# Kernel tuning notes

Hardware: AMD Instinct MI355X
Metric: run time of the kernel (lower is better)

## Reference

```python
import jax, jax.numpy as jnp
import numpy as np

N_NODES = 50000
N_GRAPHS = 64
HID = 128
IN_DIM = 128
N_LAYERS = 3


def setup_inputs() -> dict:
    key = jax.random.key(0)
    ks = jax.random.split(key, 12)
    x = jax.random.normal(ks[0], (N_NODES, IN_DIM), dtype=jnp.float32)
    edge_index = jax.random.randint(ks[1], (2, 800000), 0, N_NODES, dtype=jnp.int64)
    batch = jnp.sort(jax.random.randint(ks[2], (N_NODES,), 0, N_GRAPHS, dtype=jnp.int64))
    s = 1.0 / np.sqrt(HID)
    W0 = jax.random.normal(ks[3], (IN_DIM, HID), dtype=jnp.float32) * s
    b0 = jnp.zeros((HID,), dtype=jnp.float32)
    Ws = jax.random.normal(ks[4], (N_LAYERS, HID, HID), dtype=jnp.float32) * s
    bs = jnp.zeros((N_LAYERS, HID), dtype=jnp.float32)
    W1 = jax.random.normal(ks[5], (HID, HID // 2), dtype=jnp.float32) * s
    b1 = jnp.zeros((HID // 2,), dtype=jnp.float32)
    W2 = jax.random.normal(ks[6], (HID // 2, 2), dtype=jnp.float32) * (1.0 / np.sqrt(HID // 2))
    b2 = jnp.zeros((2,), dtype=jnp.float32)
    return {"x": x, "edge_index": edge_index, "batch": batch,
            "W0": W0, "b0": b0, "Ws": Ws, "bs": bs,
            "W1": W1, "b1": b1, "W2": W2, "b2": b2}


def reference(x, edge_index, batch, W0, b0, Ws, bs, W1, b1, W2, b2):
    n = x.shape[0]
    # GCN: add self-loops, symmetric normalization D^-1/2 (A+I) D^-1/2
    loop = jnp.arange(n, dtype=edge_index.dtype)
    src = jnp.concatenate([edge_index[0], loop])  # [E+N]
    dst = jnp.concatenate([edge_index[1], loop])
    deg = jax.ops.segment_sum(jnp.ones_like(dst, dtype=x.dtype), dst, num_segments=n)
    dinv = jax.lax.rsqrt(jnp.maximum(deg, 1.0))
    coef = (dinv[src] * dinv[dst])[:, None]  # [E+N, 1]

    def gcn(h, W, b):
        hw = h @ W                                  # transform first (cheaper)
        agg = jax.ops.segment_sum(hw[src] * coef, dst, num_segments=n)
        return jax.nn.relu(agg + b)

    h = gcn(x, W0, b0)
    for i in range(Ws.shape[0]):
        h = gcn(h, Ws[i], bs[i])

    # global mean pool over graphs
    sums = jax.ops.segment_sum(h, batch, num_segments=N_GRAPHS)
    cnts = jax.ops.segment_sum(jnp.ones((n,), dtype=h.dtype), batch, num_segments=N_GRAPHS)
    pooled = sums / jnp.maximum(cnts, 1.0)[:, None]  # [G, HID]

    out = jax.nn.relu(pooled @ W1 + b1) @ W2 + b2    # [G, 2]
    return out
```

## Files before the change

### kernel.cpp

```cpp
#include <hip/hip_runtime.h>
#include <hip/hip_bf16.h>
#include <hip/hip_fp16.h>

#define HID 128
#define N_GRAPHS 64

__global__ void init_deg_kernel(int* __restrict__ deg, int n) {
    int i = blockIdx.x * 256 + threadIdx.x;
    if (i < n) deg[i] = 1;
}

__global__ void count_kernel(const int* __restrict__ dst, int* __restrict__ deg, int E) {
    int e = blockIdx.x * 256 + threadIdx.x;
    if (e < E) atomicAdd(&deg[dst[e]], 1);
}

__global__ __launch_bounds__(256) void scan_partial_kernel(const int* __restrict__ deg,
                                                           int* __restrict__ bsum, int n) {
    __shared__ int red[256];
    int t = threadIdx.x;
    int i = blockIdx.x * 256 + t;
    red[t] = (i < n) ? deg[i] : 0;
    __syncthreads();
#pragma unroll
    for (int s = 128; s > 0; s >>= 1) {
        if (t < s) red[t] += red[t + s];
        __syncthreads();
    }
    if (t == 0) bsum[blockIdx.x] = red[0];
}

__global__ __launch_bounds__(256) void scan_bsum_kernel(const int* __restrict__ bsum,
                                                        int* __restrict__ boff,
                                                        int* __restrict__ row_ptr,
                                                        int nb, int n) {
    __shared__ int arr[256];
    int t = threadIdx.x;
    int own = (t < nb) ? bsum[t] : 0;
    arr[t] = own;
    __syncthreads();
#pragma unroll
    for (int off = 1; off < 256; off <<= 1) {
        int v = arr[t];
        int add = (t >= off) ? arr[t - off] : 0;
        __syncthreads();
        arr[t] = v + add;
        __syncthreads();
    }
    if (t < nb) boff[t] = arr[t] - own;
    if (t == 255) row_ptr[n] = arr[255];
}

__global__ __launch_bounds__(256) void scan_emit_kernel(const int* __restrict__ deg,
                                                        const int* __restrict__ boff,
                                                        int* __restrict__ row_ptr,
                                                        int* __restrict__ cursor,
                                                        float* __restrict__ dinv, int n) {
    __shared__ int arr[256];
    int t = threadIdx.x;
    int i = blockIdx.x * 256 + t;
    int d = (i < n) ? deg[i] : 0;
    arr[t] = d;
    __syncthreads();
#pragma unroll
    for (int off = 1; off < 256; off <<= 1) {
        int v = arr[t];
        int add = (t >= off) ? arr[t - off] : 0;
        __syncthreads();
        arr[t] = v + add;
        __syncthreads();
    }
    if (i < n) {
        int pos = boff[blockIdx.x] + arr[t] - d;
        row_ptr[i] = pos;
        cursor[i] = pos;
        dinv[i] = rsqrtf((float)d);
    }
}

__global__ void fill_kernel(const int* __restrict__ src, const int* __restrict__ dst,
                            int* __restrict__ cursor, int* __restrict__ col,
                            int E, int EN) {
    int e = blockIdx.x * 256 + threadIdx.x;
    if (e >= EN) return;
    int s, d;
    if (e < E) { s = src[e]; d = dst[e]; }
    else       { s = e - E; d = s; }
    int pos = atomicAdd(&cursor[d], 1);
    col[pos] = s;
}

__global__ __launch_bounds__(256) void gemm_scale_kernel(const float* __restrict__ A,
                                                         const float* __restrict__ W,
                                                         const float* __restrict__ dinv,
                                                         __half* __restrict__ out16, int M) {
    __shared__ float sAT[2][32][68];
    __shared__ float sW [2][32][132];
    int tid = threadIdx.x;
    int row0 = blockIdx.x * 64;
    int ty = tid >> 5, tx = tid & 31;
    int r0 = ty * 8;
    int j0 = tx * 4;

    float acc[8][4];
#pragma unroll
    for (int i = 0; i < 8; ++i)
#pragma unroll
        for (int j = 0; j < 4; ++j) acc[i][j] = 0.f;

#pragma unroll
    for (int p = 0; p < 4; ++p) {
        int idx = tid + p * 256;
        int k = idx >> 5, c4 = idx & 31;
        *(float4*)&sW[0][k][c4 * 4] = *(const float4*)(W + (size_t)k * 128 + c4 * 4);
    }
#pragma unroll
    for (int p = 0; p < 2; ++p) {
        int idx = tid + p * 256;
        int r = idx >> 3, c4 = idx & 7;
        float4 v = make_float4(0.f, 0.f, 0.f, 0.f);
        if (row0 + r < M) v = *(const float4*)(A + (size_t)(row0 + r) * 128 + c4 * 4);
        sAT[0][c4 * 4 + 0][r] = v.x;
        sAT[0][c4 * 4 + 1][r] = v.y;
        sAT[0][c4 * 4 + 2][r] = v.z;
        sAT[0][c4 * 4 + 3][r] = v.w;
    }
    __syncthreads();

    for (int kci = 0; kci < 4; ++kci) {
        int cur = kci & 1;
        float4 wreg[4], areg[2];
        if (kci < 3) {
            int kc = (kci + 1) * 32;
#pragma unroll
            for (int p = 0; p < 4; ++p) {
                int idx = tid + p * 256;
                int k = idx >> 5, c4 = idx & 31;
                wreg[p] = *(const float4*)(W + (size_t)(kc + k) * 128 + c4 * 4);
            }
#pragma unroll
            for (int p = 0; p < 2; ++p) {
                int idx = tid + p * 256;
                int r = idx >> 3, c4 = idx & 7;
                areg[p] = make_float4(0.f, 0.f, 0.f, 0.f);
                if (row0 + r < M) areg[p] = *(const float4*)(A + (size_t)(row0 + r) * 128 + kc + c4 * 4);
            }
        }

#pragma unroll 4
        for (int k = 0; k < 32; ++k) {
            float4 a0 = *(float4*)&sAT[cur][k][r0];
            float4 a1 = *(float4*)&sAT[cur][k][r0 + 4];
            float4 w4 = *(float4*)&sW[cur][k][j0];
            float a[8] = {a0.x, a0.y, a0.z, a0.w, a1.x, a1.y, a1.z, a1.w};
#pragma unroll
            for (int i = 0; i < 8; ++i) {
                acc[i][0] += a[i] * w4.x;
                acc[i][1] += a[i] * w4.y;
                acc[i][2] += a[i] * w4.z;
                acc[i][3] += a[i] * w4.w;
            }
        }
        __syncthreads();

        if (kci < 3) {
            int nbuf = cur ^ 1;
#pragma unroll
            for (int p = 0; p < 4; ++p) {
                int idx = tid + p * 256;
                int k = idx >> 5, c4 = idx & 31;
                *(float4*)&sW[nbuf][k][c4 * 4] = wreg[p];
            }
#pragma unroll
            for (int p = 0; p < 2; ++p) {
                int idx = tid + p * 256;
                int r = idx >> 3, c4 = idx & 7;
                sAT[nbuf][c4 * 4 + 0][r] = areg[p].x;
                sAT[nbuf][c4 * 4 + 1][r] = areg[p].y;
                sAT[nbuf][c4 * 4 + 2][r] = areg[p].z;
                sAT[nbuf][c4 * 4 + 3][r] = areg[p].w;
            }
            __syncthreads();
        }
    }

#pragma unroll
    for (int i = 0; i < 8; ++i) {
        int r = row0 + r0 + i;
        if (r < M) {
            float dv = dinv[r];
            __half2 h0 = __floats2half2_rn(acc[i][0] * dv, acc[i][1] * dv);
            __half2 h1 = __floats2half2_rn(acc[i][2] * dv, acc[i][3] * dv);
            float2 pk;
            ((__half2*)&pk)[0] = h0; ((__half2*)&pk)[1] = h1;
            *(float2*)(out16 + (size_t)r * 128 + j0) = pk;
        }
    }
}

__global__ __launch_bounds__(256) void aggregate_kernel(const __half* __restrict__ hw,
                                                        const int* __restrict__ row_ptr,
                                                        const int* __restrict__ col,
                                                        const float* __restrict__ dinv,
                                                        const float* __restrict__ bias,
                                                        float* __restrict__ out, int n) {
    int tid = threadIdx.x;
    int v = blockIdx.x * 16 + (tid >> 4);
    if (v >= n) return;
    int j = (tid & 15) * 8;
    int p0 = row_ptr[v], p1 = row_ptr[v + 1];
    float acc[8];
#pragma unroll
    for (int q = 0; q < 8; ++q) acc[q] = 0.f;

    int p = p0;
    for (; p + 3 < p1; p += 4) {
        int s0 = col[p], s1 = col[p + 1], s2 = col[p + 2], s3 = col[p + 3];
        float4 r0 = *(const float4*)(hw + (size_t)s0 * 128 + j);
        float4 r1 = *(const float4*)(hw + (size_t)s1 * 128 + j);
        float4 r2 = *(const float4*)(hw + (size_t)s2 * 128 + j);
        float4 r3 = *(const float4*)(hw + (size_t)s3 * 128 + j);
        const __half2* h0 = (const __half2*)&r0;
        const __half2* h1 = (const __half2*)&r1;
        const __half2* h2 = (const __half2*)&r2;
        const __half2* h3 = (const __half2*)&r3;
#pragma unroll
        for (int q = 0; q < 4; ++q) {
            float2 f0 = __half22float2(h0[q]);
            float2 f1 = __half22float2(h1[q]);
            float2 f2 = __half22float2(h2[q]);
            float2 f3 = __half22float2(h3[q]);
            acc[2 * q + 0] += (f0.x + f1.x) + (f2.x + f3.x);
            acc[2 * q + 1] += (f0.y + f1.y) + (f2.y + f3.y);
        }
    }
    for (; p < p1; ++p) {
        int s0 = col[p];
        float4 r0 = *(const float4*)(hw + (size_t)s0 * 128 + j);
        const __half2* h0 = (const __half2*)&r0;
#pragma unroll
        for (int q = 0; q < 4; ++q) {
            float2 f0 = __half22float2(h0[q]);
            acc[2 * q + 0] += f0.x;
            acc[2 * q + 1] += f0.y;
        }
    }
    float dv = dinv[v];
    float4 bb0 = *(const float4*)(bias + j);
    float4 bb1 = *(const float4*)(bias + j + 4);
    float4 o0, o1;
    o0.x = fmaxf(acc[0] * dv + bb0.x, 0.f);
    o0.y = fmaxf(acc[1] * dv + bb0.y, 0.f);
    o0.z = fmaxf(acc[2] * dv + bb0.z, 0.f);
    o0.w = fmaxf(acc[3] * dv + bb0.w, 0.f);
    o1.x = fmaxf(acc[4] * dv + bb1.x, 0.f);
    o1.y = fmaxf(acc[5] * dv + bb1.y, 0.f);
    o1.z = fmaxf(acc[6] * dv + bb1.z, 0.f);
    o1.w = fmaxf(acc[7] * dv + bb1.w, 0.f);
    *(float4*)(out + (size_t)v * 128 + j) = o0;
    *(float4*)(out + (size_t)v * 128 + j + 4) = o1;
}

__global__ void boundary_kernel(const int* __restrict__ batch, int* __restrict__ start, int n) {
    int i = blockIdx.x * 256 + threadIdx.x;
    if (i >= n) return;
    int b = batch[i];
    int pb = (i > 0) ? batch[i - 1] : -1;
    if (b != pb) {
        for (int g = pb + 1; g <= b; ++g) start[g] = i;
    }
    if (i == n - 1) {
        for (int g = b + 1; g <= N_GRAPHS; ++g) start[g] = n;
    }
}

__global__ __launch_bounds__(256) void pool_reduce_kernel(const float* __restrict__ h,
                                                          const int* __restrict__ start,
                                                          float* __restrict__ pooled) {
    __shared__ float part[8][128];
    int g = blockIdx.x;
    int s = start[g], e = start[g + 1];
    int tid = threadIdx.x;
    int grp = tid >> 5;
    int j = (tid & 31) * 4;
    float4 acc = make_float4(0.f, 0.f, 0.f, 0.f);
    for (int v = s + grp; v < e; v += 8) {
        float4 a = *(const float4*)(h + (size_t)v * 128 + j);
        acc.x += a.x; acc.y += a.y; acc.z += a.z; acc.w += a.w;
    }
    *(float4*)&part[grp][j] = acc;
    __syncthreads();
    if (tid < 128) {
        float sum = 0.f;
#pragma unroll
        for (int k = 0; k < 8; ++k) sum += part[k][tid];
        int cntv = e - s; if (cntv < 1) cntv = 1;
        pooled[g * 128 + tid] = sum / (float)cntv;
    }
}

__global__ __launch_bounds__(256) void mlp_kernel(const float* __restrict__ pooled_g,
                                                  const float* __restrict__ W1,
                                                  const float* __restrict__ b1,
                                                  const float* __restrict__ W2,
                                                  const float* __restrict__ b2,
                                                  float* __restrict__ out) {
    __shared__ float pooled[64][128];
    __shared__ float h1[64][64];
    int tid = threadIdx.x;
    for (int i = tid; i < 64 * 128; i += 256) pooled[i >> 7][i & 127] = pooled_g[i];
    __syncthreads();
    for (int i = tid; i < 64 * 64; i += 256) {
        int g = i >> 6, j = i & 63;
        float acc = b1[j];
        for (int k = 0; k < 128; ++k) acc += pooled[g][k] * W1[k * 64 + j];
        h1[g][j] = fmaxf(acc, 0.f);
    }
    __syncthreads();
    if (tid < 128) {
        int g = tid >> 1, c = tid & 1;
        float acc = b2[c];
        for (int jj = 0; jj < 64; ++jj) acc += h1[g][jj] * W2[jj * 2 + c];
        out[tid] = acc;
    }
}

extern "C" void kernel_launch(void* const* d_in, const int* in_sizes, int n_in,
                              void* d_out, int out_size, void* d_ws, size_t ws_size,
                              hipStream_t stream) {
    const float* x    = (const float*)d_in[0];
    const int*   ei   = (const int*)d_in[1];
    const int*   batch= (const int*)d_in[2];
    const float* W0   = (const float*)d_in[3];
    const float* b0   = (const float*)d_in[4];
    const float* Ws   = (const float*)d_in[5];
    const float* bs   = (const float*)d_in[6];
    const float* W1   = (const float*)d_in[7];
    const float* b1   = (const float*)d_in[8];
    const float* W2   = (const float*)d_in[9];
    const float* b2   = (const float*)d_in[10];
    float* out = (float*)d_out;

    const int n  = in_sizes[0] / HID;
    const int E  = in_sizes[1] / 2;
    const int EN = E + n;
    const int* src = ei;
    const int* dst = ei + E;
    const int nb = (n + 255) / 256;

    char* ws = (char*)d_ws;
    size_t off = 0;
    auto alloc = [&](size_t bytes) { void* p = ws + off; off = (off + bytes + 255) & ~(size_t)255; return p; };
    float*  bufA   = (float*) alloc((size_t)n * HID * 4);
    __half* hw16   = (__half*)alloc((size_t)n * HID * 2);
    float*  dinv   = (float*) alloc((size_t)n * 4);
    int*    row_ptr= (int*)   alloc((size_t)(n + 1) * 4);
    int*    cursor = (int*)   alloc((size_t)n * 4);
    int*    deg    = (int*)   alloc((size_t)n * 4);
    int*    col    = (int*)   alloc((size_t)EN * 4);
    int*    bsum   = (int*)   alloc((size_t)nb * 4);
    int*    boff   = (int*)   alloc((size_t)nb * 4);
    int*    gstart = (int*)   alloc((N_GRAPHS + 1) * 4);
    float*  pooled = (float*) alloc(N_GRAPHS * 128 * 4);
    (void)ws_size; (void)n_in; (void)out_size;

    init_deg_kernel<<<nb, 256, 0, stream>>>(deg, n);
    count_kernel<<<(E + 255) / 256, 256, 0, stream>>>(dst, deg, E);
    scan_partial_kernel<<<nb, 256, 0, stream>>>(deg, bsum, n);
    scan_bsum_kernel<<<1, 256, 0, stream>>>(bsum, boff, row_ptr, nb, n);
    scan_emit_kernel<<<nb, 256, 0, stream>>>(deg, boff, row_ptr, cursor, dinv, n);
    fill_kernel<<<(EN + 255) / 256, 256, 0, stream>>>(src, dst, cursor, col, E, EN);
    boundary_kernel<<<nb, 256, 0, stream>>>(batch, gstart, n);

    const int gemm_grid = (n + 63) / 64;
    const int node_grid = (n + 15) / 16;

    gemm_scale_kernel<<<gemm_grid, 256, 0, stream>>>(x, W0, dinv, hw16, n);
    aggregate_kernel<<<node_grid, 256, 0, stream>>>(hw16, row_ptr, col, dinv, b0, bufA, n);
    for (int l = 0; l < 3; ++l) {
        gemm_scale_kernel<<<gemm_grid, 256, 0, stream>>>(bufA, Ws + (size_t)l * HID * HID, dinv, hw16, n);
        aggregate_kernel<<<node_grid, 256, 0, stream>>>(hw16, row_ptr, col, dinv, bs + (size_t)l * HID, bufA, n);
    }

    pool_reduce_kernel<<<N_GRAPHS, 256, 0, stream>>>(bufA, gstart, pooled);
    mlp_kernel<<<1, 256, 0, stream>>>(pooled, W1, b1, W2, b2, out);
}
```

Before: 511.0 us.

## Use fp16 MFMA for node transforms and store activations in half precision

Replaces the fp32 SIMT tiled GEMM with a matrix-core kernel using mfma_f32_16x16x32_f16. W is transposed and converted to fp16 in shared memory, and each wave computes 16 rows. Layer activations are now stored as fp16, so the aggregate output, the GEMM input and the pooling all read and write half the bytes, and a conversion kernel turns x into fp16 up front. This costs precision through fp16 rounding of the inputs, the weights and the intermediate hidden states. The output stores are narrow 2-byte scattered writes.

Result: faster. 461.8 us (-9.6%).

```diff
diff --git a/kernel.cpp b/kernel.cpp
--- a/kernel.cpp
+++ b/kernel.cpp
@@ -4,6 +4,9 @@
 
 #define HID 128
 #define N_GRAPHS 64
+
+typedef _Float16 h8 __attribute__((ext_vector_type(8)));
+typedef float f4 __attribute__((ext_vector_type(4)));
 
 __global__ void init_deg_kernel(int* __restrict__ deg, int n) {
     int i = blockIdx.x * 256 + threadIdx.x;
@@ -90,110 +93,78 @@
     col[pos] = s;
 }
 
-__global__ __launch_bounds__(256) void gemm_scale_kernel(const float* __restrict__ A,
-                                                         const float* __restrict__ W,
-                                                         const float* __restrict__ dinv,
-                                                         __half* __restrict__ out16, int M) {
-    __shared__ float sAT[2][32][68];
-    __shared__ float sW [2][32][132];
+__global__ void cvt_kernel(const float* __restrict__ in, __half* __restrict__ out, int total8) {
+    int i = blockIdx.x * 256 + threadIdx.x;
+    if (i >= total8) return;
+    float4 v0 = *(const float4*)(in + (size_t)i * 8);
+    float4 v1 = *(const float4*)(in + (size_t)i * 8 + 4);
+    __half2 p0 = __floats2half2_rn(v0.x, v0.y);
+    __half2 p1 = __floats2half2_rn(v0.z, v0.w);
+    __half2 p2 = __floats2half2_rn(v1.x, v1.y);
+    __half2 p3 = __floats2half2_rn(v1.z, v1.w);
+    float4 pk;
+    ((__half2*)&pk)[0] = p0; ((__half2*)&pk)[1] = p1;
+    ((__half2*)&pk)[2] = p2; ((__half2*)&pk)[3] = p3;
+    *(float4*)(out + (size_t)i * 8) = pk;
+}
+
+__global__ __launch_bounds__(256) void gemm_mfma_kernel(const __half* __restrict__ A16,
+                                                        const float* __restrict__ W,
+                                                        const float* __restrict__ dinv,
+                                                        __half* __restrict__ out16, int M) {
+    __shared__ _Float16 sWt[128][136];
     int tid = threadIdx.x;
-    int row0 = blockIdx.x * 64;
-    int ty = tid >> 5, tx = tid & 31;
-    int r0 = ty * 8;
-    int j0 = tx * 4;
-
-    float acc[8][4];
-#pragma unroll
-    for (int i = 0; i < 8; ++i)
-#pragma unroll
-        for (int j = 0; j < 4; ++j) acc[i][j] = 0.f;
-
-#pragma unroll
-    for (int p = 0; p < 4; ++p) {
-        int idx = tid + p * 256;
-        int k = idx >> 5, c4 = idx & 31;
-        *(float4*)&sW[0][k][c4 * 4] = *(const float4*)(W + (size_t)k * 128 + c4 * 4);
-    }
-#pragma unroll
-    for (int p = 0; p < 2; ++p) {
-        int idx = tid + p * 256;
-        int r = idx >> 3, c4 = idx & 7;
-        float4 v = make_float4(0.f, 0.f, 0.f, 0.f);
-        if (row0 + r < M) v = *(const float4*)(A + (size_t)(row0 + r) * 128 + c4 * 4);
-        sAT[0][c4 * 4 + 0][r] = v.x;
-        sAT[0][c4 * 4 + 1][r] = v.y;
-        sAT[0][c4 * 4 + 2][r] = v.z;
-        sAT[0][c4 * 4 + 3][r] = v.w;
-    }
-    __syncthreads();
-
-    for (int kci = 0; kci < 4; ++kci) {
-        int cur = kci & 1;
-        float4 wreg[4], areg[2];
-        if (kci < 3) {
-            int kc = (kci + 1) * 32;
-#pragma unroll
-            for (int p = 0; p < 4; ++p) {
-                int idx = tid + p * 256;
-                int k = idx >> 5, c4 = idx & 31;
-                wreg[p] = *(const float4*)(W + (size_t)(kc + k) * 128 + c4 * 4);
-            }
-#pragma unroll
-            for (int p = 0; p < 2; ++p) {
-                int idx = tid + p * 256;
-                int r = idx >> 3, c4 = idx & 7;
-                areg[p] = make_float4(0.f, 0.f, 0.f, 0.f);
-                if (row0 + r < M) areg[p] = *(const float4*)(A + (size_t)(row0 + r) * 128 + kc + c4 * 4);
-            }
-        }
-
-#pragma unroll 4
-        for (int k = 0; k < 32; ++k) {
-            float4 a0 = *(float4*)&sAT[cur][k][r0];
-            float4 a1 = *(float4*)&sAT[cur][k][r0 + 4];
-            float4 w4 = *(float4*)&sW[cur][k][j0];
-            float a[8] = {a0.x, a0.y, a0.z, a0.w, a1.x, a1.y, a1.z, a1.w};
-#pragma unroll
-            for (int i = 0; i < 8; ++i) {
-                acc[i][0] += a[i] * w4.x;
-                acc[i][1] += a[i] * w4.y;
-                acc[i][2] += a[i] * w4.z;
-                acc[i][3] += a[i] * w4.w;
-            }
-        }
-        __syncthreads();
-
-        if (kci < 3) {
-            int nbuf = cur ^ 1;
-#pragma unroll
-            for (int p = 0; p < 4; ++p) {
-                int idx = tid + p * 256;
-                int k = idx >> 5, c4 = idx & 31;
-                *(float4*)&sW[nbuf][k][c4 * 4] = wreg[p];
-            }
-#pragma unroll
-            for (int p = 0; p < 2; ++p) {
-                int idx = tid + p * 256;
-                int r = idx >> 3, c4 = idx & 7;
-                sAT[nbuf][c4 * 4 + 0][r] = areg[p].x;
-                sAT[nbuf][c4 * 4 + 1][r] = areg[p].y;
-                sAT[nbuf][c4 * 4 + 2][r] = areg[p].z;
-                sAT[nbuf][c4 * 4 + 3][r] = areg[p].w;
-            }
-            __syncthreads();
-        }
-    }
-
-#pragma unroll
-    for (int i = 0; i < 8; ++i) {
-        int r = row0 + r0 + i;
-        if (r < M) {
-            float dv = dinv[r];
-            __half2 h0 = __floats2half2_rn(acc[i][0] * dv, acc[i][1] * dv);
-            __half2 h1 = __floats2half2_rn(acc[i][2] * dv, acc[i][3] * dv);
-            float2 pk;
-            ((__half2*)&pk)[0] = h0; ((__half2*)&pk)[1] = h1;
-            *(float2*)(out16 + (size_t)r * 128 + j0) = pk;
+    for (int i = tid * 4; i < 128 * 128; i += 1024) {
+        int k = i >> 7, nn = i & 127;
+        float4 v = *(const float4*)(W + i);
+        sWt[nn + 0][k] = (_Float16)v.x;
+        sWt[nn + 1][k] = (_Float16)v.y;
+        sWt[nn + 2][k] = (_Float16)v.z;
+        sWt[nn + 3][k] = (_Float16)v.w;
+    }
+    __syncthreads();
+
+    int wave = tid >> 6;
+    int lane = tid & 63;
+    int l15 = lane & 15;
+    int kg = lane >> 4;
+    int rowb = blockIdx.x * 64 + wave * 16;
+    int arow = rowb + l15;
+
+    h8 zero;
+#pragma unroll
+    for (int q = 0; q < 8; ++q) zero[q] = (_Float16)0.f;
+
+    h8 afrag[4];
+    if (arow < M) {
+        const h8* Av = (const h8*)(A16 + (size_t)arow * 128 + kg * 8);
+#pragma unroll
+        for (int kc = 0; kc < 4; ++kc) afrag[kc] = Av[kc * 4];
+    } else {
+#pragma unroll
+        for (int kc = 0; kc < 4; ++kc) afrag[kc] = zero;
+    }
+
+    int orow0 = rowb + kg * 4;
+    float dv[4];
+#pragma unroll
+    for (int j = 0; j < 4; ++j)
+        dv[j] = (orow0 + j < M) ? dinv[orow0 + j] : 0.f;
+
+    for (int ct = 0; ct < 8; ++ct) {
+        h8 bfrag[4];
+#pragma unroll
+        for (int kc = 0; kc < 4; ++kc)
+            bfrag[kc] = *(const h8*)&sWt[ct * 16 + l15][kc * 32 + kg * 8];
+        f4 acc = {0.f, 0.f, 0.f, 0.f};
+#pragma unroll
+        for (int kc = 0; kc < 4; ++kc)
+            acc = __builtin_amdgcn_mfma_f32_16x16x32_f16(afrag[kc], bfrag[kc], acc, 0, 0, 0);
+#pragma unroll
+        for (int j = 0; j < 4; ++j) {
+            int r = orow0 + j;
+            if (r < M)
+                out16[(size_t)r * 128 + ct * 16 + l15] = __float2half(acc[j] * dv[j]);
         }
     }
 }
@@ -203,7 +174,7 @@
                                                         const int* __restrict__ col,
                                                         const float* __restrict__ dinv,
                                                         const float* __restrict__ bias,
-                                                        float* __restrict__ out, int n) {
+                                                        __half* __restrict__ out16, int n) {
     int tid = threadIdx.x;
     int v = blockIdx.x * 16 + (tid >> 4);
     if (v >= n) return;
@@ -248,17 +219,21 @@
     float dv = dinv[v];
     float4 bb0 = *(const float4*)(bias + j);
     float4 bb1 = *(const float4*)(bias + j + 4);
-    float4 o0, o1;
-    o0.x = fmaxf(acc[0] * dv + bb0.x, 0.f);
-    o0.y = fmaxf(acc[1] * dv + bb0.y, 0.f);
-    o0.z = fmaxf(acc[2] * dv + bb0.z, 0.f);
-    o0.w = fmaxf(acc[3] * dv + bb0.w, 0.f);
-    o1.x = fmaxf(acc[4] * dv + bb1.x, 0.f);
-    o1.y = fmaxf(acc[5] * dv + bb1.y, 0.f);
-    o1.z = fmaxf(acc[6] * dv + bb1.z, 0.f);
-    o1.w = fmaxf(acc[7] * dv + bb1.w, 0.f);
-    *(float4*)(out + (size_t)v * 128 + j) = o0;
-    *(float4*)(out + (size_t)v * 128 + j + 4) = o1;
+    float r[8];
+    r[0] = fmaxf(acc[0] * dv + bb0.x, 0.f);
+    r[1] = fmaxf(acc[1] * dv + bb0.y, 0.f);
+    r[2] = fmaxf(acc[2] * dv + bb0.z, 0.f);
+    r[3] = fmaxf(acc[3] * dv + bb0.w, 0.f);
+    r[4] = fmaxf(acc[4] * dv + bb1.x, 0.f);
+    r[5] = fmaxf(acc[5] * dv + bb1.y, 0.f);
+    r[6] = fmaxf(acc[6] * dv + bb1.z, 0.f);
+    r[7] = fmaxf(acc[7] * dv + bb1.w, 0.f);
+    float4 pk;
+    ((__half2*)&pk)[0] = __floats2half2_rn(r[0], r[1]);
+    ((__half2*)&pk)[1] = __floats2half2_rn(r[2], r[3]);
+    ((__half2*)&pk)[2] = __floats2half2_rn(r[4], r[5]);
+    ((__half2*)&pk)[3] = __floats2half2_rn(r[6], r[7]);
+    *(float4*)(out16 + (size_t)v * 128 + j) = pk;
 }
 
 __global__ void boundary_kernel(const int* __restrict__ batch, int* __restrict__ start, int n) {
@@ -274,7 +249,7 @@
     }
 }
 
-__global__ __launch_bounds__(256) void pool_reduce_kernel(const float* __restrict__ h,
+__global__ __launch_bounds__(256) void pool_reduce_kernel(const __half* __restrict__ h,
                                                           const int* __restrict__ start,
                                                           float* __restrict__ pooled) {
     __shared__ float part[8][128];
@@ -285,8 +260,10 @@
     int j = (tid & 31) * 4;
     float4 acc = make_float4(0.f, 0.f, 0.f, 0.f);
     for (int v = s + grp; v < e; v += 8) {
-        float4 a = *(const float4*)(h + (size_t)v * 128 + j);
-        acc.x += a.x; acc.y += a.y; acc.z += a.z; acc.w += a.w;
+        float2 raw = *(const float2*)(h + (size_t)v * 128 + j);
+        float2 f0 = __half22float2(((const __half2*)&raw)[0]);
+        float2 f1 = __half22float2(((const __half2*)&raw)[1]);
+        acc.x += f0.x; acc.y += f0.y; acc.z += f1.x; acc.w += f1.y;
     }
     *(float4*)&part[grp][j] = acc;
     __syncthreads();
@@ -351,7 +328,7 @@
     char* ws = (char*)d_ws;
     size_t off = 0;
     auto alloc = [&](size_t bytes) { void* p = ws + off; off = (off + bytes + 255) & ~(size_t)255; return p; };
-    float*  bufA   = (float*) alloc((size_t)n * HID * 4);
+    __half* h16    = (__half*)alloc((size_t)n * HID * 2);
     __half* hw16   = (__half*)alloc((size_t)n * HID * 2);
     float*  dinv   = (float*) alloc((size_t)n * 4);
     int*    row_ptr= (int*)   alloc((size_t)(n + 1) * 4);
@@ -371,17 +348,18 @@
     scan_emit_kernel<<<nb, 256, 0, stream>>>(deg, boff, row_ptr, cursor, dinv, n);
     fill_kernel<<<(EN + 255) / 256, 256, 0, stream>>>(src, dst, cursor, col, E, EN);
     boundary_kernel<<<nb, 256, 0, stream>>>(batch, gstart, n);
+    cvt_kernel<<<(n * HID / 8 + 255) / 256, 256, 0, stream>>>(x, h16, n * HID / 8);
 
     const int gemm_grid = (n + 63) / 64;
     const int node_grid = (n + 15) / 16;
 
-    gemm_scale_kernel<<<gemm_grid, 256, 0, stream>>>(x, W0, dinv, hw16, n);
-    aggregate_kernel<<<node_grid, 256, 0, stream>>>(hw16, row_ptr, col, dinv, b0, bufA, n);
+    gemm_mfma_kernel<<<gemm_grid, 256, 0, stream>>>(h16, W0, dinv, hw16, n);
+    aggregate_kernel<<<node_grid, 256, 0, stream>>>(hw16, row_ptr, col, dinv, b0, h16, n);
     for (int l = 0; l < 3; ++l) {
-        gemm_scale_kernel<<<gemm_grid, 256, 0, stream>>>(bufA, Ws + (size_t)l * HID * HID, dinv, hw16, n);
-        aggregate_kernel<<<node_grid, 256, 0, stream>>>(hw16, row_ptr, col, dinv, bs + (size_t)l * HID, bufA, n);
-    }
-
-    pool_reduce_kernel<<<N_GRAPHS, 256, 0, stream>>>(bufA, gstart, pooled);
+        gemm_mfma_kernel<<<gemm_grid, 256, 0, stream>>>(h16, Ws + (size_t)l * HID * HID, dinv, hw16, n);
+        aggregate_kernel<<<node_grid, 256, 0, stream>>>(hw16, row_ptr, col, dinv, bs + (size_t)l * HID, h16, n);
+    }
+
+    pool_reduce_kernel<<<N_GRAPHS, 256, 0, stream>>>(h16, gstart, pooled);
     mlp_kernel<<<1, 256, 0, stream>>>(pooled, W1, b1, W2, b2, out);
 }
```
